# Optimization experiments

Measured on AMD Instinct MI355X. Metric: run time of the kernel, lower is better.

Reference implementation:

```python
import jax, jax.numpy as jnp
import numpy as np

N_NODES = 100000
N_EDGES = 1280000
D_IN = 64
D_HID = 64
D_OUT = 64


def sage_conv(x, src, dst, W_l, b_l, W_r):
    # PyG SAGEConv (aggr='mean', root_weight=True):
    #   out_i = W_l @ mean_{j in N(i)} x_j + b_l + W_r @ x_i
    msg = x[src]  # [E, d] gather of source-node features
    agg = jax.ops.segment_sum(msg, dst, num_segments=N_NODES)
    cnt = jax.ops.segment_sum(jnp.ones((src.shape[0],), x.dtype), dst,
                              num_segments=N_NODES)
    mean = agg / jnp.maximum(cnt, 1.0)[:, None]
    return mean @ W_l.T + b_l + x @ W_r.T


def setup_inputs() -> dict:
    key = jax.random.key(0)
    ks = jax.random.split(key, 8)
    x = jax.random.normal(ks[0], (N_NODES, D_IN), dtype=jnp.float32)
    edge_index = jax.random.randint(ks[1], (2, N_EDGES), 0, N_NODES,
                                    dtype=jnp.int64)
    s1 = 1.0 / np.sqrt(D_IN)
    s2 = 1.0 / np.sqrt(D_HID)
    W1_l = jax.random.uniform(ks[2], (D_HID, D_IN), jnp.float32, -s1, s1)
    b1 = jnp.zeros((D_HID,), jnp.float32)
    W1_r = jax.random.uniform(ks[3], (D_HID, D_IN), jnp.float32, -s1, s1)
    W2_l = jax.random.uniform(ks[4], (D_OUT, D_HID), jnp.float32, -s2, s2)
    b2 = jnp.zeros((D_OUT,), jnp.float32)
    W2_r = jax.random.uniform(ks[5], (D_OUT, D_HID), jnp.float32, -s2, s2)
    return {"x": x, "edge_index": edge_index,
            "W1_l": W1_l, "b1": b1, "W1_r": W1_r,
            "W2_l": W2_l, "b2": b2, "W2_r": W2_r}


def reference(x, edge_index, W1_l, b1, W1_r, W2_l, b2, W2_r):
    src, dst = edge_index[0], edge_index[1]
    h = sage_conv(x, src, dst, W1_l, b1, W1_r)
    h = jax.nn.relu(h)
    # dropout p=0.0 -> identity
    out = sage_conv(h, src, dst, W2_l, b2, W2_r)
    return out
```

## Files before the change

kernel.cpp:

```cpp
#include <hip/hip_runtime.h>

#define NN 100000
#define NE 1280000
#define D  64

#define BINSZ   512
#define NBIN    196
#define ESTRIDE 7168
#define CHUNK   4096
#define NT      (NN / 16)

typedef unsigned int   uint;
typedef unsigned short ushort;
typedef unsigned char  uchar;
typedef __attribute__((ext_vector_type(8))) short short8v;
typedef __attribute__((ext_vector_type(4))) float f32x4;

__device__ __forceinline__ ushort f2bf(float f) {
    uint u = __float_as_uint(f);
    uint r = (u + 0x7fffu + ((u >> 16) & 1u)) >> 16;
    return (ushort)r;
}
__device__ __forceinline__ float bf2f(ushort h) {
    return __uint_as_float(((uint)h) << 16);
}
__device__ __forceinline__ float bfhi_f(uint w) { return __uint_as_float(w & 0xffff0000u); }
__device__ __forceinline__ float bflo_f(uint w) { return __uint_as_float(w << 16); }

__global__ __launch_bounds__(256) void prep_x(const float* __restrict__ x,
                                              uint* __restrict__ xb) {
    int i = blockIdx.x * 256 + threadIdx.x;
    if (i < NN * 32) {
        float2 v = ((const float2*)x)[i];
        xb[i] = (uint)f2bf(v.x) | ((uint)f2bf(v.y) << 16);
    }
}

__global__ __launch_bounds__(256) void prep_w(const float* __restrict__ w0,
                                              const float* __restrict__ w1,
                                              const float* __restrict__ w2,
                                              const float* __restrict__ w3,
                                              ushort* __restrict__ hi,
                                              ushort* __restrict__ lo) {
    int g = blockIdx.x * 256 + threadIdx.x;
    if (g < 4 * 4096) {
        int m = g >> 12;
        const float* src = (m == 0) ? w0 : (m == 1) ? w1 : (m == 2) ? w2 : w3;
        float f = src[g & 4095];
        ushort h = f2bf(f);
        hi[g] = h;
        lo[g] = f2bf(f - bf2f(h));
    }
}

__global__ __launch_bounds__(256) void bin_scatter(const int* __restrict__ srcv,
                                                   const int* __restrict__ dstv,
                                                   int* __restrict__ bincur,
                                                   uint* __restrict__ ecol) {
    __shared__ uint  ebuf[CHUNK];
    __shared__ uchar bbuf[CHUNK];
    __shared__ int hist[256];
    __shared__ int hbase[256];
    __shared__ int cur[256];
    __shared__ int gbase[256];

    const int tid  = threadIdx.x;
    const int base = blockIdx.x * CHUNK;

    hist[tid] = 0;
    __syncthreads();

    uint pk[16];
    int  bn[16];
    #pragma unroll
    for (int r = 0; r < 16; ++r) {
        const int e = base + r * 256 + tid;
        if (e < NE) {
            const int d = dstv[e];
            bn[r] = d >> 9;
            pk[r] = ((uint)srcv[e] << 9) | (uint)(d & 511);
            atomicAdd(&hist[bn[r]], 1);
        } else {
            bn[r] = -1;
        }
    }
    __syncthreads();

    int v = hist[tid];
    hbase[tid] = v;
    __syncthreads();
    for (int d = 1; d < 256; d <<= 1) {
        int t = (tid >= d) ? hbase[tid - d] : 0;
        __syncthreads();
        hbase[tid] += t;
        __syncthreads();
    }
    const int excl = hbase[tid] - v;
    hbase[tid] = excl;
    cur[tid]   = excl;
    __syncthreads();

    #pragma unroll
    for (int r = 0; r < 16; ++r) {
        if (bn[r] >= 0) {
            const int p = atomicAdd(&cur[bn[r]], 1);
            ebuf[p] = pk[r];
            bbuf[p] = (uchar)bn[r];
        }
    }
    if (tid < NBIN && hist[tid] > 0)
        gbase[tid] = atomicAdd(&bincur[tid], hist[tid]);
    __syncthreads();

    const int n = min(CHUNK, NE - base);
    for (int i = tid; i < n; i += 256) {
        const int b   = bbuf[i];
        const int pib = gbase[b] + (i - hbase[b]);
        if (pib < ESTRIDE)
            ecol[(size_t)b * ESTRIDE + pib] = ebuf[i];
    }
}

__global__ __launch_bounds__(256) void binscan(const int* __restrict__ bincur,
                                               int* __restrict__ binbase,
                                               int* __restrict__ offs) {
    __shared__ int buf[256];
    const int t = threadIdx.x;
    int v = (t < NBIN) ? min(bincur[t], ESTRIDE) : 0;
    buf[t] = v;
    __syncthreads();
    for (int d = 1; d < 256; d <<= 1) {
        int tv = (t >= d) ? buf[t - d] : 0;
        __syncthreads();
        buf[t] += tv;
        __syncthreads();
    }
    if (t < NBIN) binbase[t] = buf[t] - v;
    if (t == 0) {
        binbase[NBIN] = buf[255];
        offs[NN]      = buf[255];
    }
}

__global__ __launch_bounds__(1024) void binsort(const uint* __restrict__ ecol,
                                                const int* __restrict__ bincur,
                                                const int* __restrict__ binbase,
                                                int* __restrict__ col,
                                                int* __restrict__ offs) {
    __shared__ int hist[512];
    __shared__ int cnt_[512];
    __shared__ int cur[512];
    __shared__ int colbuf[ESTRIDE];

    const int b = blockIdx.x;
    const int t = threadIdx.x;
    const int n    = min(bincur[b], ESTRIDE);
    const int gsrc = b * ESTRIDE;
    const int gdst = binbase[b];

    if (t < 512) hist[t] = 0;
    __syncthreads();

    for (int i = t; i < n; i += 1024)
        atomicAdd(&hist[ecol[gsrc + i] & 511], 1);
    __syncthreads();

    if (t < 512) cnt_[t] = hist[t];
    __syncthreads();
    for (int d = 1; d < 512; d <<= 1) {
        int tv = (t >= d && t < 512) ? hist[t - d] : 0;
        __syncthreads();
        if (t < 512) hist[t] += tv;
        __syncthreads();
    }
    if (t < 512) {
        const int excl = hist[t] - cnt_[t];
        cur[t] = excl;
        const int node = b * BINSZ + t;
        if (node < NN) offs[node] = gdst + excl;
    }
    __syncthreads();

    for (int i = t; i < n; i += 1024) {
        const uint e = ecol[gsrc + i];
        const int  p = atomicAdd(&cur[e & 511], 1);
        colbuf[p] = (int)(e >> 9);
    }
    __syncthreads();

    for (int i = t; i < n; i += 1024)
        col[gdst + i] = colbuf[i];
}

template<int SELF_BF16, int WF32, int WB16>
__global__ __launch_bounds__(256) void fused_layer(
        const uint*   __restrict__ gsrc,
        const float*  __restrict__ selff,
        const ushort* __restrict__ selfb,
        const int*    __restrict__ col,
        const int*    __restrict__ offs,
        const ushort* __restrict__ wl_hi, const ushort* __restrict__ wl_lo,
        const ushort* __restrict__ wr_hi, const ushort* __restrict__ wr_lo,
        const float*  __restrict__ bias,
        float* __restrict__ outf, ushort* __restrict__ outb,
        int do_relu)
{
    const int l   = threadIdx.x & 63;
    const int wid = (blockIdx.x * 256 + threadIdx.x) >> 6;
    if (wid >= NT) return;
    const int m16  = l & 15;
    const int q    = l >> 4;
    const int koff = q * 8;
    const int mbase = wid * 16;
    const int node  = mbase + m16;

    const int o0  = offs[node];
    const int deg = offs[node + 1] - o0;

    float acc[16];
    #pragma unroll
    for (int j = 0; j < 16; ++j) acc[j] = 0.f;

    for (int k0 = 0;; k0 += 4) {
        if (!__any(k0 < deg)) break;
        int id[4];
        #pragma unroll
        for (int u = 0; u < 4; ++u) {
            const int k = k0 + u;
            id[u] = (k < deg) ? col[o0 + k] : -1;
        }
        uint4 r0[4], r1[4];
        #pragma unroll
        for (int u = 0; u < 4; ++u) {
            if (id[u] >= 0) {
                const uint* row = gsrc + (size_t)id[u] * 32;
                r0[u] = *(const uint4*)(row + 4 * q);
                r1[u] = *(const uint4*)(row + 16 + 4 * q);
            }
        }
        #pragma unroll
        for (int u = 0; u < 4; ++u) {
            if (id[u] >= 0) {
                uint w;
                w = r0[u].x; acc[0]  += bflo_f(w); acc[1]  += bfhi_f(w);
                w = r0[u].y; acc[2]  += bflo_f(w); acc[3]  += bfhi_f(w);
                w = r0[u].z; acc[4]  += bflo_f(w); acc[5]  += bfhi_f(w);
                w = r0[u].w; acc[6]  += bflo_f(w); acc[7]  += bfhi_f(w);
                w = r1[u].x; acc[8]  += bflo_f(w); acc[9]  += bfhi_f(w);
                w = r1[u].y; acc[10] += bflo_f(w); acc[11] += bfhi_f(w);
                w = r1[u].z; acc[12] += bflo_f(w); acc[13] += bfhi_f(w);
                w = r1[u].w; acc[14] += bflo_f(w); acc[15] += bfhi_f(w);
            }
        }
    }

    const float inv = 1.0f / (float)max(deg, 1);
    short8v am[2];
    #pragma unroll
    for (int j = 0; j < 8; ++j) {
        am[0][j] = (short)f2bf(acc[j] * inv);
        am[1][j] = (short)f2bf(acc[8 + j] * inv);
    }

    short8v ashi[2], aslo[2];
    if (SELF_BF16) {
        ashi[0] = *(const short8v*)(selfb + (size_t)node * 64 + koff);
        ashi[1] = *(const short8v*)(selfb + (size_t)node * 64 + 32 + koff);
    } else {
        #pragma unroll
        for (int kk = 0; kk < 2; ++kk) {
            const float4* xp = (const float4*)(selff + (size_t)node * 64 + kk * 32 + koff);
            float4 v0 = xp[0], v1 = xp[1];
            float vv[8] = {v0.x, v0.y, v0.z, v0.w, v1.x, v1.y, v1.z, v1.w};
            #pragma unroll
            for (int j = 0; j < 8; ++j) {
                ushort hb_ = f2bf(vv[j]);
                ashi[kk][j] = (short)hb_;
                aslo[kk][j] = (short)f2bf(vv[j] - bf2f(hb_));
            }
        }
    }

    #pragma unroll
    for (int nt = 0; nt < 4; ++nt) {
        f32x4 acc4 = {0.f, 0.f, 0.f, 0.f};
        #pragma unroll
        for (int kk = 0; kk < 2; ++kk) {
            const size_t wo = (size_t)(nt * 16 + m16) * 64 + kk * 32 + koff;
            short8v bwlh = *(const short8v*)(wl_hi + wo);
            short8v bwll = *(const short8v*)(wl_lo + wo);
            short8v bwrh = *(const short8v*)(wr_hi + wo);
            short8v bwrl = *(const short8v*)(wr_lo + wo);
            acc4 = __builtin_amdgcn_mfma_f32_16x16x32_bf16(am[kk],   bwlh, acc4, 0, 0, 0);
            acc4 = __builtin_amdgcn_mfma_f32_16x16x32_bf16(am[kk],   bwll, acc4, 0, 0, 0);
            acc4 = __builtin_amdgcn_mfma_f32_16x16x32_bf16(ashi[kk], bwrh, acc4, 0, 0, 0);
            if (!SELF_BF16)
                acc4 = __builtin_amdgcn_mfma_f32_16x16x32_bf16(aslo[kk], bwrh, acc4, 0, 0, 0);
            acc4 = __builtin_amdgcn_mfma_f32_16x16x32_bf16(ashi[kk], bwrl, acc4, 0, 0, 0);
        }
        const float bv = bias[nt * 16 + m16];
        #pragma unroll
        for (int r = 0; r < 4; ++r) {
            float v = acc4[r] + bv;
            if (do_relu) v = fmaxf(v, 0.f);
            const size_t oi = (size_t)(mbase + q * 4 + r) * 64 + nt * 16 + m16;
            if (WF32) outf[oi] = v;
            if (WB16) outb[oi] = f2bf(v);
        }
    }
}

extern "C" void kernel_launch(void* const* d_in, const int* in_sizes, int n_in,
                              void* d_out, int out_size, void* d_ws, size_t ws_size,
                              hipStream_t stream) {
    const float* x   = (const float*)d_in[0];
    const int*   ei  = (const int*)d_in[1];
    const float* W1l = (const float*)d_in[2];
    const float* b1  = (const float*)d_in[3];
    const float* W1r = (const float*)d_in[4];
    const float* W2l = (const float*)d_in[5];
    const float* b2  = (const float*)d_in[6];
    const float* W2r = (const float*)d_in[7];
    float*       out = (float*)d_out;

    const int* src = ei;
    const int* dst = ei + NE;

    char* p = (char*)d_ws;
    int*    bincur  = (int*)p;    p += 1024;
    int*    binbase = (int*)p;    p += 1024;
    int*    col     = (int*)p;    p += (size_t)NE * 4;
    int*    offs    = (int*)p;    p += (size_t)(NN + 1) * 4 + 60;
    ushort* whi     = (ushort*)p; p += (size_t)4 * 4096 * 2;
    ushort* wlo     = (ushort*)p; p += (size_t)4 * 4096 * 2;
    uint*   xb      = (uint*)p;   p += (size_t)NN * 32 * 4;
    uint*   hb      = (uint*)p;   p += (size_t)NN * 32 * 4;
    uint*   ecol    = hb;

    const ushort* w1l_hi = whi;             const ushort* w1l_lo = wlo;
    const ushort* w1r_hi = whi + 4096;      const ushort* w1r_lo = wlo + 4096;
    const ushort* w2l_hi = whi + 2 * 4096;  const ushort* w2l_lo = wlo + 2 * 4096;
    const ushort* w2r_hi = whi + 3 * 4096;  const ushort* w2r_lo = wlo + 3 * 4096;

    hipMemsetAsync(bincur, 0, 1024, stream);

    prep_x<<<(NN * 32 + 255) / 256, 256, 0, stream>>>(x, xb);
    prep_w<<<(4 * 4096 + 255) / 256, 256, 0, stream>>>(W1l, W1r, W2l, W2r, whi, wlo);

    bin_scatter<<<(NE + CHUNK - 1) / CHUNK, 256, 0, stream>>>(src, dst, bincur, ecol);
    binscan<<<1, 256, 0, stream>>>(bincur, binbase, offs);
    binsort<<<NBIN, 1024, 0, stream>>>(ecol, bincur, binbase, col, offs);

    fused_layer<0, 0, 1><<<(NT * 64 + 255) / 256, 256, 0, stream>>>(
        xb, x, nullptr, col, offs,
        w1l_hi, w1l_lo, w1r_hi, w1r_lo, b1, nullptr, (ushort*)hb, 1);

    fused_layer<1, 1, 0><<<(NT * 64 + 255) / 256, 256, 0, stream>>>(
        hb, nullptr, (const ushort*)hb, col, offs,
        w2l_hi, w2l_lo, w2r_hi, w2r_lo, b2, out, nullptr, 0);
}
```

Measured before the change: 249.8 us.

## Merge prep kernels, drop binscan, register-resident binsort, double-buffer neighbor gathers

Merges the x and weight conversion kernels into one launch that converts x with wider 8-float vector loads. Removes the separate binscan kernel: each binsort block sums the preceding bin counts itself, and the shared-memory colbuf staging is replaced by writing directly from registers using atomic ranks. bin_scatter reuses the atomic return value as a rank instead of a second atomic pass. The aggregation loop in fused_layer is double-buffered so the next neighbor gather is issued while the current one is consumed, with nontemporal loads for col and nontemporal output stores. The changes cut launch overhead and are meant to hide gather latency, at the cost of more registers and redundant prefix sums in every binsort block.

```diff
diff --git a/kernel.cpp b/kernel.cpp
--- a/kernel.cpp
+++ b/kernel.cpp
@@ -26,30 +26,40 @@
 }
 __device__ __forceinline__ float bfhi_f(uint w) { return __uint_as_float(w & 0xffff0000u); }
 __device__ __forceinline__ float bflo_f(uint w) { return __uint_as_float(w << 16); }
-
-__global__ __launch_bounds__(256) void prep_x(const float* __restrict__ x,
-                                              uint* __restrict__ xb) {
-    int i = blockIdx.x * 256 + threadIdx.x;
-    if (i < NN * 32) {
-        float2 v = ((const float2*)x)[i];
-        xb[i] = (uint)f2bf(v.x) | ((uint)f2bf(v.y) << 16);
-    }
-}
-
-__global__ __launch_bounds__(256) void prep_w(const float* __restrict__ w0,
-                                              const float* __restrict__ w1,
-                                              const float* __restrict__ w2,
-                                              const float* __restrict__ w3,
-                                              ushort* __restrict__ hi,
-                                              ushort* __restrict__ lo) {
-    int g = blockIdx.x * 256 + threadIdx.x;
-    if (g < 4 * 4096) {
-        int m = g >> 12;
-        const float* src = (m == 0) ? w0 : (m == 1) ? w1 : (m == 2) ? w2 : w3;
-        float f = src[g & 4095];
-        ushort h = f2bf(f);
-        hi[g] = h;
-        lo[g] = f2bf(f - bf2f(h));
+__device__ __forceinline__ uint packbf(float a, float b) {
+    return (uint)f2bf(a) | ((uint)f2bf(b) << 16);
+}
+
+#define XBLKS 3125
+__global__ __launch_bounds__(256) void prep(const float* __restrict__ x,
+                                            uint* __restrict__ xb,
+                                            const float* __restrict__ w0,
+                                            const float* __restrict__ w1,
+                                            const float* __restrict__ w2,
+                                            const float* __restrict__ w3,
+                                            ushort* __restrict__ hi,
+                                            ushort* __restrict__ lo) {
+    const int bid = blockIdx.x;
+    if (bid < XBLKS) {
+        const int g = bid * 256 + threadIdx.x;
+        const float4* xp = (const float4*)x + (size_t)g * 2;
+        const float4 v0 = xp[0], v1 = xp[1];
+        uint4 o;
+        o.x = packbf(v0.x, v0.y);
+        o.y = packbf(v0.z, v0.w);
+        o.z = packbf(v1.x, v1.y);
+        o.w = packbf(v1.z, v1.w);
+        ((uint4*)xb)[g] = o;
+    } else {
+        const int g = (bid - XBLKS) * 256 + threadIdx.x;
+        if (g < 4 * 4096) {
+            const int m = g >> 12;
+            const float* src = (m == 0) ? w0 : (m == 1) ? w1 : (m == 2) ? w2 : w3;
+            const float f = src[g & 4095];
+            const ushort h = f2bf(f);
+            hi[g] = h;
+            lo[g] = f2bf(f - bf2f(h));
+        }
     }
 }
 
@@ -61,7 +71,6 @@
     __shared__ uchar bbuf[CHUNK];
     __shared__ int hist[256];
     __shared__ int hbase[256];
-    __shared__ int cur[256];
     __shared__ int gbase[256];
 
     const int tid  = threadIdx.x;
@@ -71,7 +80,7 @@
     __syncthreads();
 
     uint pk[16];
-    int  bn[16];
+    int  bn[16], rk[16];
     #pragma unroll
     for (int r = 0; r < 16; ++r) {
         const int e = base + r * 256 + tid;
@@ -79,37 +88,35 @@
             const int d = dstv[e];
             bn[r] = d >> 9;
             pk[r] = ((uint)srcv[e] << 9) | (uint)(d & 511);
-            atomicAdd(&hist[bn[r]], 1);
+            rk[r] = atomicAdd(&hist[bn[r]], 1);
         } else {
             bn[r] = -1;
         }
     }
     __syncthreads();
 
-    int v = hist[tid];
+    const int v = hist[tid];
     hbase[tid] = v;
     __syncthreads();
     for (int d = 1; d < 256; d <<= 1) {
-        int t = (tid >= d) ? hbase[tid - d] : 0;
+        const int t = (tid >= d) ? hbase[tid - d] : 0;
         __syncthreads();
         hbase[tid] += t;
         __syncthreads();
     }
-    const int excl = hbase[tid] - v;
-    hbase[tid] = excl;
-    cur[tid]   = excl;
+    hbase[tid] -= v;
+    if (tid < NBIN && v > 0)
+        gbase[tid] = atomicAdd(&bincur[tid], v);
     __syncthreads();
 
     #pragma unroll
     for (int r = 0; r < 16; ++r) {
         if (bn[r] >= 0) {
-            const int p = atomicAdd(&cur[bn[r]], 1);
+            const int p = hbase[bn[r]] + rk[r];
             ebuf[p] = pk[r];
             bbuf[p] = (uchar)bn[r];
         }
     }
-    if (tid < NBIN && hist[tid] > 0)
-        gbase[tid] = atomicAdd(&bincur[tid], hist[tid]);
     __syncthreads();
 
     const int n = min(CHUNK, NE - base);
@@ -121,75 +128,104 @@
     }
 }
 
-__global__ __launch_bounds__(256) void binscan(const int* __restrict__ bincur,
-                                               int* __restrict__ binbase,
-                                               int* __restrict__ offs) {
-    __shared__ int buf[256];
-    const int t = threadIdx.x;
-    int v = (t < NBIN) ? min(bincur[t], ESTRIDE) : 0;
-    buf[t] = v;
-    __syncthreads();
-    for (int d = 1; d < 256; d <<= 1) {
-        int tv = (t >= d) ? buf[t - d] : 0;
-        __syncthreads();
-        buf[t] += tv;
-        __syncthreads();
-    }
-    if (t < NBIN) binbase[t] = buf[t] - v;
-    if (t == 0) {
-        binbase[NBIN] = buf[255];
-        offs[NN]      = buf[255];
-    }
-}
-
 __global__ __launch_bounds__(1024) void binsort(const uint* __restrict__ ecol,
                                                 const int* __restrict__ bincur,
-                                                const int* __restrict__ binbase,
                                                 int* __restrict__ col,
                                                 int* __restrict__ offs) {
     __shared__ int hist[512];
     __shared__ int cnt_[512];
-    __shared__ int cur[512];
-    __shared__ int colbuf[ESTRIDE];
+    __shared__ int gdst_s;
 
     const int b = blockIdx.x;
     const int t = threadIdx.x;
     const int n    = min(bincur[b], ESTRIDE);
     const int gsrc = b * ESTRIDE;
-    const int gdst = binbase[b];
 
     if (t < 512) hist[t] = 0;
-    __syncthreads();
-
-    for (int i = t; i < n; i += 1024)
-        atomicAdd(&hist[ecol[gsrc + i] & 511], 1);
-    __syncthreads();
-
-    if (t < 512) cnt_[t] = hist[t];
+    if (t < 64) {
+        int s = 0;
+        for (int i = t; i < b; i += 64) s += min(bincur[i], ESTRIDE);
+        #pragma unroll
+        for (int d = 1; d < 64; d <<= 1) s += __shfl_xor(s, d);
+        if (t == 0) gdst_s = s;
+    }
+    __syncthreads();
+    const int gdst = gdst_s;
+
+    const int NIT = ESTRIDE / 1024;
+    int nd[NIT], ee[NIT], rk[NIT];
+    #pragma unroll
+    for (int it = 0; it < NIT; ++it) {
+        const int i = t + it * 1024;
+        if (i < n) {
+            const uint e = ecol[gsrc + i];
+            nd[it] = (int)(e & 511);
+            ee[it] = (int)(e >> 9);
+            rk[it] = atomicAdd(&hist[nd[it]], 1);
+        } else {
+            nd[it] = -1;
+        }
+    }
+    __syncthreads();
+
+    int v = 0;
+    if (t < 512) { v = hist[t]; cnt_[t] = v; }
     __syncthreads();
     for (int d = 1; d < 512; d <<= 1) {
-        int tv = (t >= d && t < 512) ? hist[t - d] : 0;
+        const int tv = (t >= d && t < 512) ? hist[t - d] : 0;
         __syncthreads();
         if (t < 512) hist[t] += tv;
         __syncthreads();
     }
     if (t < 512) {
         const int excl = hist[t] - cnt_[t];
-        cur[t] = excl;
+        hist[t] = excl;
         const int node = b * BINSZ + t;
         if (node < NN) offs[node] = gdst + excl;
-    }
-    __syncthreads();
-
-    for (int i = t; i < n; i += 1024) {
-        const uint e = ecol[gsrc + i];
-        const int  p = atomicAdd(&cur[e & 511], 1);
-        colbuf[p] = (int)(e >> 9);
-    }
-    __syncthreads();
-
-    for (int i = t; i < n; i += 1024)
-        col[gdst + i] = colbuf[i];
+        if (b == NBIN - 1 && node == NN - 1) offs[NN] = gdst + n;
+    }
+    __syncthreads();
+
+    #pragma unroll
+    for (int it = 0; it < NIT; ++it)
+        if (nd[it] >= 0)
+            col[gdst + hist[nd[it]] + rk[it]] = ee[it];
+}
+
+__device__ __forceinline__ void gload(int (&id)[4], uint4 (&r0)[4], uint4 (&r1)[4],
+                                      int k0, int deg, const int* __restrict__ col,
+                                      int o0, const uint* __restrict__ gsrc, int q) {
+    #pragma unroll
+    for (int u = 0; u < 4; ++u) {
+        const int k = k0 + u;
+        id[u] = (k < deg) ? __builtin_nontemporal_load(col + o0 + k) : -1;
+    }
+    #pragma unroll
+    for (int u = 0; u < 4; ++u) {
+        if (id[u] >= 0) {
+            const uint* row = gsrc + (size_t)id[u] * 32;
+            r0[u] = *(const uint4*)(row + 4 * q);
+            r1[u] = *(const uint4*)(row + 16 + 4 * q);
+        }
+    }
+}
+
+__device__ __forceinline__ void gconsume(const int (&id)[4], const uint4 (&r0)[4],
+                                         const uint4 (&r1)[4], float (&acc)[16]) {
+    #pragma unroll
+    for (int u = 0; u < 4; ++u) {
+        if (id[u] >= 0) {
+            uint w;
+            w = r0[u].x; acc[0]  += bflo_f(w); acc[1]  += bfhi_f(w);
+            w = r0[u].y; acc[2]  += bflo_f(w); acc[3]  += bfhi_f(w);
+            w = r0[u].z; acc[4]  += bflo_f(w); acc[5]  += bfhi_f(w);
+            w = r0[u].w; acc[6]  += bflo_f(w); acc[7]  += bfhi_f(w);
+            w = r1[u].x; acc[8]  += bflo_f(w); acc[9]  += bfhi_f(w);
+            w = r1[u].y; acc[10] += bflo_f(w); acc[11] += bfhi_f(w);
+            w = r1[u].z; acc[12] += bflo_f(w); acc[13] += bfhi_f(w);
+            w = r1[u].w; acc[14] += bflo_f(w); acc[15] += bfhi_f(w);
+        }
+    }
 }
 
 template<int SELF_BF16, int WF32, int WB16>
@@ -208,9 +244,9 @@
     const int l   = threadIdx.x & 63;
     const int wid = (blockIdx.x * 256 + threadIdx.x) >> 6;
     if (wid >= NT) return;
-    const int m16  = l & 15;
-    const int q    = l >> 4;
-    const int koff = q * 8;
+    const int m16   = l & 15;
+    const int q     = l >> 4;
+    const int koff  = q * 8;
     const int mbase = wid * 16;
     const int node  = mbase + m16;
 
@@ -221,36 +257,23 @@
     #pragma unroll
     for (int j = 0; j < 16; ++j) acc[j] = 0.f;
 
-    for (int k0 = 0;; k0 += 4) {
-        if (!__any(k0 < deg)) break;
-        int id[4];
-        #pragma unroll
-        for (int u = 0; u < 4; ++u) {
-            const int k = k0 + u;
-            id[u] = (k < deg) ? col[o0 + k] : -1;
-        }
-        uint4 r0[4], r1[4];
-        #pragma unroll
-        for (int u = 0; u < 4; ++u) {
-            if (id[u] >= 0) {
-                const uint* row = gsrc + (size_t)id[u] * 32;
-                r0[u] = *(const uint4*)(row + 4 * q);
-                r1[u] = *(const uint4*)(row + 16 + 4 * q);
-            }
-        }
-        #pragma unroll
-        for (int u = 0; u < 4; ++u) {
-            if (id[u] >= 0) {
-                uint w;
-                w = r0[u].x; acc[0]  += bflo_f(w); acc[1]  += bfhi_f(w);
-                w = r0[u].y; acc[2]  += bflo_f(w); acc[3]  += bfhi_f(w);
-                w = r0[u].z; acc[4]  += bflo_f(w); acc[5]  += bfhi_f(w);
-                w = r0[u].w; acc[6]  += bflo_f(w); acc[7]  += bfhi_f(w);
-                w = r1[u].x; acc[8]  += bflo_f(w); acc[9]  += bfhi_f(w);
-                w = r1[u].y; acc[10] += bflo_f(w); acc[11] += bfhi_f(w);
-                w = r1[u].z; acc[12] += bflo_f(w); acc[13] += bfhi_f(w);
-                w = r1[u].w; acc[14] += bflo_f(w); acc[15] += bfhi_f(w);
-            }
+    int idA[4], idB[4];
+    uint4 a0[4], a1[4], b0[4], b1[4];
+
+    if (__any(deg > 0)) {
+        gload(idA, a0, a1, 0, deg, col, o0, gsrc, q);
+        int k = 4;
+        for (;;) {
+            const bool more = __any(k < deg);
+            if (more) gload(idB, b0, b1, k, deg, col, o0, gsrc, q);
+            gconsume(idA, a0, a1, acc);
+            if (!more) break;
+            k += 4;
+            const bool more2 = __any(k < deg);
+            if (more2) gload(idA, a0, a1, k, deg, col, o0, gsrc, q);
+            gconsume(idB, b0, b1, acc);
+            if (!more2) break;
+            k += 4;
         }
     }
 
@@ -270,11 +293,11 @@
         #pragma unroll
         for (int kk = 0; kk < 2; ++kk) {
             const float4* xp = (const float4*)(selff + (size_t)node * 64 + kk * 32 + koff);
-            float4 v0 = xp[0], v1 = xp[1];
-            float vv[8] = {v0.x, v0.y, v0.z, v0.w, v1.x, v1.y, v1.z, v1.w};
+            const float4 v0 = xp[0], v1 = xp[1];
+            const float vv[8] = {v0.x, v0.y, v0.z, v0.w, v1.x, v1.y, v1.z, v1.w};
             #pragma unroll
             for (int j = 0; j < 8; ++j) {
-                ushort hb_ = f2bf(vv[j]);
+                const ushort hb_ = f2bf(vv[j]);
                 ashi[kk][j] = (short)hb_;
                 aslo[kk][j] = (short)f2bf(vv[j] - bf2f(hb_));
             }
@@ -287,10 +310,10 @@
         #pragma unroll
         for (int kk = 0; kk < 2; ++kk) {
             const size_t wo = (size_t)(nt * 16 + m16) * 64 + kk * 32 + koff;
-            short8v bwlh = *(const short8v*)(wl_hi + wo);
-            short8v bwll = *(const short8v*)(wl_lo + wo);
-            short8v bwrh = *(const short8v*)(wr_hi + wo);
-            short8v bwrl = *(const short8v*)(wr_lo + wo);
+            const short8v bwlh = *(const short8v*)(wl_hi + wo);
+            const short8v bwll = *(const short8v*)(wl_lo + wo);
+            const short8v bwrh = *(const short8v*)(wr_hi + wo);
+            const short8v bwrl = *(const short8v*)(wr_lo + wo);
             acc4 = __builtin_amdgcn_mfma_f32_16x16x32_bf16(am[kk],   bwlh, acc4, 0, 0, 0);
             acc4 = __builtin_amdgcn_mfma_f32_16x16x32_bf16(am[kk],   bwll, acc4, 0, 0, 0);
             acc4 = __builtin_amdgcn_mfma_f32_16x16x32_bf16(ashi[kk], bwrh, acc4, 0, 0, 0);
@@ -304,8 +327,8 @@
             float v = acc4[r] + bv;
             if (do_relu) v = fmaxf(v, 0.f);
             const size_t oi = (size_t)(mbase + q * 4 + r) * 64 + nt * 16 + m16;
-            if (WF32) outf[oi] = v;
-            if (WB16) outb[oi] = f2bf(v);
+            if (WF32) __builtin_nontemporal_store(v, &outf[oi]);
+            if (WB16) __builtin_nontemporal_store(f2bf(v), &outb[oi]);
         }
     }
 }
@@ -327,15 +350,14 @@
     const int* dst = ei + NE;
 
     char* p = (char*)d_ws;
-    int*    bincur  = (int*)p;    p += 1024;
-    int*    binbase = (int*)p;    p += 1024;
-    int*    col     = (int*)p;    p += (size_t)NE * 4;
-    int*    offs    = (int*)p;    p += (size_t)(NN + 1) * 4 + 60;
-    ushort* whi     = (ushort*)p; p += (size_t)4 * 4096 * 2;
-    ushort* wlo     = (ushort*)p; p += (size_t)4 * 4096 * 2;
-    uint*   xb      = (uint*)p;   p += (size_t)NN * 32 * 4;
-    uint*   hb      = (uint*)p;   p += (size_t)NN * 32 * 4;
-    uint*   ecol    = hb;
+    int*    bincur = (int*)p;    p += 1024;
+    int*    col    = (int*)p;    p += (size_t)NE * 4;
+    int*    offs   = (int*)p;    p += (size_t)(NN + 1) * 4 + 60;
+    ushort* whi    = (ushort*)p; p += (size_t)4 * 4096 * 2;
+    ushort* wlo    = (ushort*)p; p += (size_t)4 * 4096 * 2;
+    uint*   xb     = (uint*)p;   p += (size_t)NN * 32 * 4;
+    uint*   hb     = (uint*)p;   p += (size_t)NN * 32 * 4;
+    uint*   ecol   = hb;
 
     const ushort* w1l_hi = whi;             const ushort* w1l_lo = wlo;
     const ushort* w1r_hi = whi + 4096;      const ushort* w1r_lo = wlo + 4096;
@@ -344,12 +366,10 @@
 
     hipMemsetAsync(bincur, 0, 1024, stream);
 
-    prep_x<<<(NN * 32 + 255) / 256, 256, 0, stream>>>(x, xb);
-    prep_w<<<(4 * 4096 + 255) / 256, 256, 0, stream>>>(W1l, W1r, W2l, W2r, whi, wlo);
+    prep<<<XBLKS + 64, 256, 0, stream>>>(x, xb, W1l, W1r, W2l, W2r, whi, wlo);
 
     bin_scatter<<<(NE + CHUNK - 1) / CHUNK, 256, 0, stream>>>(src, dst, bincur, ecol);
-    binscan<<<1, 256, 0, stream>>>(bincur, binbase, offs);
-    binsort<<<NBIN, 1024, 0, stream>>>(ecol, bincur, binbase, col, offs);
+    binsort<<<NBIN, 1024, 0, stream>>>(ecol, bincur, col, offs);
 
     fused_layer<0, 0, 1><<<(NT * 64 + 255) / 256, 256, 0, stream>>>(
         xb, x, nullptr, col, offs,
```

Result: slower. 257.6 us (+3.1%).
